# Kernel optimization log

Measured on AMD Instinct MI355X. Metric: run time of the kernel, lower is better.

The kernel has to match this reference:

```python
import jax, jax.numpy as jnp
import numpy as np

EPS = 1e-5

def _ln(x, g, b):
    mu = jnp.mean(x, axis=-1, keepdims=True)
    var = jnp.mean(jnp.square(x - mu), axis=-1, keepdims=True)
    return (x - mu) * jax.lax.rsqrt(var + EPS) * g + b

def setup_inputs() -> dict:
    B, T, D, E, H, M = 2, 2048, 1024, 8, 512, 2048
    key = jax.random.key(0)
    ks = jax.random.split(key, 24)
    s = 0.02
    inp = {}
    inp['x'] = jax.random.normal(ks[0], (B, T, D), jnp.float32)
    flat = jnp.arange(M, dtype=jnp.int32) * 2  # unique token ids over B*T
    inp['index_b'] = flat // T
    inp['index_t'] = flat % T
    # shared SwiGLU (hidden = H)
    inp['sw1'] = jax.random.normal(ks[1], (H, D), jnp.float32) * s
    inp['sb1'] = jnp.zeros((H,), jnp.float32)
    inp['sw2'] = jax.random.normal(ks[2], (H, D), jnp.float32) * s
    inp['sb2'] = jnp.zeros((H,), jnp.float32)
    inp['sw3'] = jax.random.normal(ks[3], (D, H), jnp.float32) * s
    inp['sb3'] = jnp.zeros((D,), jnp.float32)
    inp['s_ln_g'] = jnp.ones((H,), jnp.float32)
    inp['s_ln_b'] = jnp.zeros((H,), jnp.float32)
    # gates
    inp['sg_w'] = jax.random.normal(ks[4], (1, D), jnp.float32) * s
    inp['sg_b'] = jnp.zeros((1,), jnp.float32)
    inp['eg_w'] = jax.random.normal(ks[5], (E, D), jnp.float32) * s
    inp['eg_b'] = jnp.zeros((E,), jnp.float32)
    inp['exp_bias'] = jnp.zeros((E,), jnp.float32)
    # per-expert SwiGLU stacks
    inp['ew1'] = jax.random.normal(ks[6], (E, H, D), jnp.float32) * s
    inp['eb1'] = jnp.zeros((E, H), jnp.float32)
    inp['ew2'] = jax.random.normal(ks[7], (E, H, D), jnp.float32) * s
    inp['eb2'] = jnp.zeros((E, H), jnp.float32)
    inp['ew3'] = jax.random.normal(ks[8], (E, D, H), jnp.float32) * s
    inp['eb3'] = jnp.zeros((E, D), jnp.float32)
    inp['sel_ln_g'] = jnp.ones((H,), jnp.float32)
    inp['sel_ln_b'] = jnp.zeros((H,), jnp.float32)
    return inp

def _forward(x, index_b, index_t, sw1, sb1, sw2, sb2, sw3, sb3, s_ln_g, s_ln_b,
             sg_w, sg_b, eg_w, eg_b, exp_bias, ew1, eb1, ew2, eb2, ew3, eb3,
             sel_ln_g, sel_ln_b):
    # shared SwiGLU over all tokens: [B,T,D]
    x1 = jnp.einsum('btd,hd->bth', x, sw1) + sb1
    x2 = jnp.einsum('btd,hd->bth', x, sw2) + sb2
    sh = _ln(jax.nn.silu(x1) * x2, s_ln_g, s_ln_b)
    shared_out = jnp.einsum('bth,dh->btd', sh, sw3) + sb3
    # MoE tokens
    x_moe = x[index_b, index_t]  # [M,D]
    shared_scores = jax.nn.sigmoid(x_moe @ sg_w.T + sg_b)       # [M,1]
    expert_scores = jax.nn.sigmoid(x_moe @ eg_w.T + eg_b)       # [M,E]
    top1_idx = jnp.argmax(expert_scores + exp_bias, axis=-1)    # [M]
    top1_score = jnp.take_along_axis(expert_scores, top1_idx[:, None], axis=-1)  # [M,1]
    weights = jax.nn.softmax(jnp.concatenate([shared_scores, top1_score], axis=-1), axis=-1)
    shared_w, expert_w = weights[:, 0], weights[:, 1]
    shared_moe_out = shared_out[index_b, index_t] * shared_w[:, None]
    # per-expert SwiGLU computed densely for all E, then token selects its expert
    h1 = jnp.einsum('md,ehd->meh', x_moe, ew1) + eb1  # [M,E,H]
    h2 = jnp.einsum('md,ehd->meh', x_moe, ew2) + eb2
    z = _ln(jax.nn.silu(h1) * h2, sel_ln_g, sel_ln_b)
    out_all = jnp.einsum('meh,edh->med', z, ew3) + eb3  # [M,E,D]
    expert_out = jnp.take_along_axis(out_all, top1_idx[:, None, None], axis=1)[:, 0]  # [M,D]
    expert_moe_out = expert_out * expert_w[:, None]
    final_out = shared_out.at[index_b, index_t].set(shared_moe_out + expert_moe_out)
    return final_out

def reference(x, index_b, index_t, sw1, sb1, sw2, sb2, sw3, sb3, s_ln_g, s_ln_b,
              sg_w, sg_b, eg_w, eg_b, exp_bias, ew1, eb1, ew2, eb2, ew3, eb3,
              sel_ln_g, sel_ln_b):
    return _forward(x, index_b, index_t, sw1, sb1, sw2, sb2, sw3, sb3, s_ln_g, s_ln_b,
                    sg_w, sg_b, eg_w, eg_b, exp_bias, ew1, eb1, ew2, eb2, ew3, eb3,
                    sel_ln_g, sel_ln_b)
```

## Files before the change

kernel.cpp:

```cpp
#include <hip/hip_runtime.h>
#include <cstdint>

typedef unsigned short u16;
typedef __bf16 bf16x8 __attribute__((ext_vector_type(8)));
typedef float f32x4 __attribute__((ext_vector_type(4)));

#define T_SEQ  2048
#define D_DIM  1024
#define H_DIM  512
#define E_NUM  8
#define M_TOK  2048
#define BT_TOK 4096
#define MAXP   3072
#define NSPLIT_NONE (1 << 28)

static __device__ __forceinline__ u16 f2bf(float f) {
    union { float f; uint32_t u; } v; v.f = f;
    uint32_t u = v.u;
    return (u16)((u + 0x7FFFu + ((u >> 16) & 1u)) >> 16);
}
static __device__ __forceinline__ uint32_t pack2(float a, float b) {
    return (uint32_t)f2bf(a) | ((uint32_t)f2bf(b) << 16);
}

static __device__ __forceinline__ void gl_lds16(const u16* g, u16* l) {
    __builtin_amdgcn_global_load_lds(
        (const __attribute__((address_space(1))) uint32_t*)g,
        (__attribute__((address_space(3))) uint32_t*)l, 16, 0, 0);
}

__global__ __launch_bounds__(256)
void cvt_all_kernel(const float* __restrict__ x,
                    const float* __restrict__ sw1, const float* __restrict__ sw2,
                    const float* __restrict__ sw3,
                    const float* __restrict__ ew1, const float* __restrict__ ew2,
                    const float* __restrict__ ew3,
                    u16* __restrict__ xb,
                    u16* __restrict__ sw1b, u16* __restrict__ sw2b, u16* __restrict__ sw3b,
                    u16* __restrict__ ew1b, u16* __restrict__ ew2b, u16* __restrict__ ew3b)
{
    long i = (long)blockIdx.x * 256 + threadIdx.x;
    const float* s; u16* d; long off;
    if      (i < 1048576) { s = x;   d = xb;   off = i; }
    else if (i < 1179648) { s = sw1; d = sw1b; off = i - 1048576; }
    else if (i < 1310720) { s = sw2; d = sw2b; off = i - 1179648; }
    else if (i < 1441792) { s = sw3; d = sw3b; off = i - 1310720; }
    else if (i < 2490368) { s = ew1; d = ew1b; off = i - 1441792; }
    else if (i < 3538944) { s = ew2; d = ew2b; off = i - 2490368; }
    else                  { s = ew3; d = ew3b; off = i - 3538944; }
    float4 v = ((const float4*)s)[off];
    uint2 o;
    o.x = pack2(v.x, v.y);
    o.y = pack2(v.z, v.w);
    ((uint2*)d)[off] = o;
}


__device__ __forceinline__ void gating_body(
    int m,
    const float* __restrict__ x,
    const int* __restrict__ ib, const int* __restrict__ itx,
    const float* __restrict__ sgw, const float* __restrict__ sgb,
    const float* __restrict__ egw, const float* __restrict__ egb,
    const float* __restrict__ ebias,
    float* __restrict__ shw, float* __restrict__ expw,
    int* __restrict__ top1, int* __restrict__ rowidx,
    float* xs, float* sc)
{
    int tid = threadIdx.x;
    int row = ib[m] * T_SEQ + itx[m];
    if (tid == 0) rowidx[m] = row;
    const float* xr = x + (size_t)row * D_DIM;
    ((float4*)xs)[tid] = ((const float4*)xr)[tid];
    __syncthreads();
    int lane = tid & 63, w = tid >> 6;
    for (int sidx = w; sidx < 9; sidx += 4) {
        const float* wr = (sidx == 0) ? sgw : (egw + (size_t)(sidx - 1) * D_DIM);
        float acc = 0.f;
        for (int i = lane; i < D_DIM; i += 64) acc += xs[i] * wr[i];
        #pragma unroll
        for (int o = 32; o > 0; o >>= 1) acc += __shfl_xor(acc, o);
        if (lane == 0) sc[sidx] = acc;
    }
    __syncthreads();
    if (tid == 0) {
        float ss = 1.f / (1.f + expf(-(sc[0] + sgb[0])));
        float es[E_NUM];
        float best = -1e30f; int bi = 0;
        #pragma unroll
        for (int e = 0; e < E_NUM; ++e) {
            es[e] = 1.f / (1.f + expf(-(sc[1 + e] + egb[e])));
            float t = es[e] + ebias[e];
            if (t > best) { best = t; bi = e; }
        }
        float ts = es[bi];
        shw[m]  = 1.f / (1.f + expf(ts - ss));
        expw[m] = 1.f / (1.f + expf(ss - ts));
        top1[m] = bi;
    }
}

__device__ __forceinline__ void bucket_body(
    const int* __restrict__ top1,
    int* __restrict__ base, int* __restrict__ cnt, int* __restrict__ perm,
    int* sm)
{
    int* lc  = sm;
    int* lb  = sm + E_NUM;
    int* cur = sm + 2 * E_NUM + 1;
    int tid = threadIdx.x;
    if (tid < E_NUM) { lc[tid] = 0; cur[tid] = 0; }
    __syncthreads();
    for (int m = tid; m < M_TOK; m += 256) atomicAdd(&lc[top1[m]], 1);
    __syncthreads();
    if (tid == 0) {
        int bacc = 0;
        for (int e = 0; e < E_NUM; ++e) { lb[e] = bacc; bacc += (lc[e] + 63) & ~63; }
        lb[E_NUM] = bacc;
    }
    __syncthreads();
    for (int m = tid; m < M_TOK; m += 256) {
        int e = top1[m];
        int pos = lb[e] + atomicAdd(&cur[e], 1);
        perm[pos] = m;
    }
    if (tid <= E_NUM) base[tid] = lb[tid];
    if (tid < E_NUM)  cnt[tid]  = lc[tid];
}

template<bool SEL>
__device__ __forceinline__ void ln_body(
    int m,
    const float* __restrict__ X,
    const float* __restrict__ g, const float* __restrict__ b,
    u16* __restrict__ out,
    const int* __restrict__ base, const int* __restrict__ cnt,
    float* red)
{
    int tid = threadIdx.x;
    if (SEL) {
        bool valid = false;
        int tot = base[E_NUM];
        if (m < tot) {
            int e = 0;
            while (!(m >= base[e] && m < base[e + 1])) ++e;
            valid = (m - base[e]) < cnt[e];
        }
        if (!valid) {
            out[(size_t)m * H_DIM + tid] = 0;
            out[(size_t)m * H_DIM + tid + 256] = 0;
            return;
        }
    }
    const float* row = X + (size_t)m * D_DIM;
    float a0 = row[tid],       c0 = row[H_DIM + tid];
    float a1 = row[tid + 256], c1 = row[H_DIM + tid + 256];
    float v0 = (a0 / (1.f + expf(-a0))) * c0;
    float v1 = (a1 / (1.f + expf(-a1))) * c1;
    float s = v0 + v1, s2 = v0 * v0 + v1 * v1;
    #pragma unroll
    for (int o = 32; o > 0; o >>= 1) {
        s  += __shfl_xor(s, o);
        s2 += __shfl_xor(s2, o);
    }
    int w = tid >> 6;
    if ((tid & 63) == 0) { red[w] = s; red[4 + w] = s2; }
    __syncthreads();
    s  = red[0] + red[1] + red[2] + red[3];
    s2 = red[4] + red[5] + red[6] + red[7];
    float mu  = s * (1.f / H_DIM);
    float var = s2 * (1.f / H_DIM) - mu * mu;
    float inv = rsqrtf(var + 1e-5f);
    out[(size_t)m * H_DIM + tid]       = f2bf((v0 - mu) * inv * g[tid] + b[tid]);
    out[(size_t)m * H_DIM + tid + 256] = f2bf((v1 - mu) * inv * g[tid + 256] + b[tid + 256]);
}

template<int MODE, int KLEN>
__device__ __forceinline__ void gemm_body(
    int bn, int bm,
    const u16* __restrict__ A, int lda,
    const u16* __restrict__ W0, const u16* __restrict__ W1, int nsplit,
    const float* __restrict__ b0, const float* __restrict__ b1,
    float* __restrict__ C,
    const int* __restrict__ base, const int* __restrict__ cnt,
    const int* __restrict__ perm, const int* __restrict__ rowidx,
    const float* __restrict__ shw, const float* __restrict__ expw,
    u16* lds)
{
    constexpr int NITER = KLEN / 64;
    const int tid   = threadIdx.x;
    const int mbase = bm * 64;

    int pend = 0;
    if (MODE >= 2) {
        const int tot = base[E_NUM];
        if (mbase >= tot) return;
        int e = 0;
        while (!(mbase >= base[e] && mbase < base[e + 1])) ++e;
        pend = base[e] + cnt[e];
        if (mbase >= pend) return;
        const size_t wstride = (size_t)H_DIM * D_DIM;
        W0 += (size_t)e * wstride;
        if (MODE == 2) W1 += (size_t)e * wstride;
        b0 += e * ((MODE == 2) ? H_DIM : D_DIM);
        if (MODE == 2) b1 += e * H_DIM;
    }

    const int w  = tid >> 6;
    const int l  = tid & 63;
    const int sr = tid >> 3;
    const int sc = tid & 7;

    const u16* agp[2];
    #pragma unroll
    for (int t = 0; t < 2; ++t) {
        int r = t * 32 + sr;
        int grow;
        if (MODE == 2) {
            int p  = mbase + r;
            int pp = (p < pend) ? p : (pend - 1);
            grow = rowidx[perm[pp]];
        } else {
            grow = mbase + r;
        }
        agp[t] = A + (size_t)grow * lda + (sc ^ (r & 7)) * 8;
    }
    const u16* bgp[4];
    #pragma unroll
    for (int t = 0; t < 4; ++t) {
        int r = t * 32 + sr;
        int n = bn * 128 + r;
        bgp[t] = ((n < nsplit) ? (W0 + (size_t)n * KLEN)
                               : (W1 + (size_t)(n - nsplit) * KLEN)) + (sc ^ (r & 7)) * 8;
    }

    const int l16 = l & 15, quad = l >> 4;
    const int wm = w >> 1, wn = w & 1;

    int avo[2][2], bvo[4][2];
    #pragma unroll
    for (int i = 0; i < 2; ++i) {
        int R = wm * 32 + i * 16 + l16;
        #pragma unroll
        for (int kx = 0; kx < 2; ++kx)
            avo[i][kx] = R * 128 + (((kx * 4 + quad) ^ (R & 7)) * 16);
    }
    #pragma unroll
    for (int j = 0; j < 4; ++j) {
        int R = wn * 64 + j * 16 + l16;
        #pragma unroll
        for (int kx = 0; kx < 2; ++kx)
            bvo[j][kx] = 8192 + R * 128 + (((kx * 4 + quad) ^ (R & 7)) * 16);
    }

    f32x4 acc[2][4];
    #pragma unroll
    for (int i = 0; i < 2; ++i)
        #pragma unroll
        for (int j = 0; j < 4; ++j)
            acc[i][j] = (f32x4){0.f, 0.f, 0.f, 0.f};

    const int kstart = (bm + bn * 3) & (NITER - 1);
    const char* ldsc = (const char*)lds;

    for (int it = 0; it < NITER; ++it) {
        int k0 = ((it + kstart) & (NITER - 1)) * 64;
        #pragma unroll
        for (int t = 0; t < 2; ++t)
            gl_lds16(agp[t] + k0, lds + t * 2048 + w * 512);
        #pragma unroll
        for (int t = 0; t < 4; ++t)
            gl_lds16(bgp[t] + k0, lds + 4096 + t * 2048 + w * 512);
        __syncthreads();
        #pragma unroll
        for (int kx = 0; kx < 2; ++kx) {
            bf16x8 av[2], bv[4];
            #pragma unroll
            for (int i = 0; i < 2; ++i)
                av[i] = *(const bf16x8*)(ldsc + avo[i][kx]);
            #pragma unroll
            for (int j = 0; j < 4; ++j)
                bv[j] = *(const bf16x8*)(ldsc + bvo[j][kx]);
            #pragma unroll
            for (int i = 0; i < 2; ++i)
                #pragma unroll
                for (int j = 0; j < 4; ++j)
                    acc[i][j] = __builtin_amdgcn_mfma_f32_16x16x32_bf16(av[i], bv[j], acc[i][j], 0, 0, 0);
        }
        __syncthreads();
    }

    if (MODE == 3) {
        #pragma unroll
        for (int i = 0; i < 2; ++i) {
            #pragma unroll
            for (int rr = 0; rr < 4; ++rr) {
                int p = mbase + wm * 32 + i * 16 + quad * 4 + rr;
                if (p < pend) {
                    int tok = perm[p];
                    int row = rowidx[tok];
                    float sw = shw[tok], ew = expw[tok];
                    float* outr = C + (size_t)row * D_DIM;
                    #pragma unroll
                    for (int j = 0; j < 4; ++j) {
                        int gn = bn * 128 + wn * 64 + j * 16 + l16;
                        outr[gn] = outr[gn] * sw + (acc[i][j][rr] + b0[gn]) * ew;
                    }
                }
            }
        }
    } else {
        #pragma unroll
        for (int i = 0; i < 2; ++i) {
            #pragma unroll
            for (int rr = 0; rr < 4; ++rr) {
                int gm = mbase + wm * 32 + i * 16 + quad * 4 + rr;
                float* outr = C + (size_t)gm * D_DIM;
                #pragma unroll
                for (int j = 0; j < 4; ++j) {
                    int gn = bn * 128 + wn * 64 + j * 16 + l16;
                    float bias = (gn < nsplit) ? b0[gn] : b1[gn - nsplit];
                    outr[gn] = acc[i][j][rr] + bias;
                }
            }
        }
    }
}


__global__ __launch_bounds__(256, 4)
void k_g1_gating(const u16* __restrict__ xb,
                 const u16* __restrict__ sw1b, const u16* __restrict__ sw2b,
                 const float* __restrict__ sb1, const float* __restrict__ sb2,
                 float* __restrict__ x12,
                 const float* __restrict__ x,
                 const int* __restrict__ ib, const int* __restrict__ itx,
                 const float* __restrict__ sgw, const float* __restrict__ sgb,
                 const float* __restrict__ egw, const float* __restrict__ egb,
                 const float* __restrict__ ebias,
                 float* __restrict__ shw, float* __restrict__ expw,
                 int* __restrict__ top1, int* __restrict__ rowidx)
{
    __shared__ __align__(16) u16 lds[(64 + 128) * 64];
    int bx = blockIdx.x;
    if (bx < 512) {
        gemm_body<0, 1024>(bx & 7, bx >> 3, xb, D_DIM, sw1b, sw2b, H_DIM, sb1, sb2, x12,
                           nullptr, nullptr, nullptr, nullptr, nullptr, nullptr, lds);
    } else {
        float* xs = (float*)lds;
        float* sc = xs + D_DIM;
        gating_body(bx - 512, x, ib, itx, sgw, sgb, egw, egb, ebias,
                    shw, expw, top1, rowidx, xs, sc);
    }
}

__global__ __launch_bounds__(256)
void k_ln_bucket(const float* __restrict__ x12,
                 const float* __restrict__ g, const float* __restrict__ b,
                 u16* __restrict__ shn,
                 const int* __restrict__ top1,
                 int* __restrict__ basep, int* __restrict__ cntp, int* __restrict__ perm)
{
    __shared__ __align__(16) float smf[32];
    int bx = blockIdx.x;
    if (bx < BT_TOK) ln_body<false>(bx, x12, g, b, shn, nullptr, nullptr, smf);
    else             bucket_body(top1, basep, cntp, perm, (int*)smf);
}

__global__ __launch_bounds__(256, 4)
void k_g2_e1(const u16* __restrict__ shn, const u16* __restrict__ sw3b,
             const float* __restrict__ sb3, float* __restrict__ out,
             const u16* __restrict__ xb,
             const u16* __restrict__ ew1b, const u16* __restrict__ ew2b,
             const float* __restrict__ eb1, const float* __restrict__ eb2,
             float* __restrict__ h12,
             const int* __restrict__ basep, const int* __restrict__ cntp,
             const int* __restrict__ perm, const int* __restrict__ rowidx)
{
    __shared__ __align__(16) u16 lds[(64 + 128) * 64];
    int bx = blockIdx.x;
    if (bx < 512) {
        gemm_body<1, 512>(bx & 7, bx >> 3, shn, H_DIM, sw3b, sw3b, NSPLIT_NONE, sb3, sb3, out,
                          nullptr, nullptr, nullptr, nullptr, nullptr, nullptr, lds);
    } else {
        int b2 = bx - 512;
        gemm_body<2, 1024>(b2 & 7, b2 >> 3, xb, D_DIM, ew1b, ew2b, H_DIM, eb1, eb2, h12,
                           basep, cntp, perm, rowidx, nullptr, nullptr, lds);
    }
}

__global__ __launch_bounds__(256)
void k_ln_sel(const float* __restrict__ h12,
              const float* __restrict__ g, const float* __restrict__ b,
              u16* __restrict__ z,
              const int* __restrict__ basep, const int* __restrict__ cntp)
{
    __shared__ __align__(16) float smf[8];
    ln_body<true>(blockIdx.x, h12, g, b, z, basep, cntp, smf);
}

__global__ __launch_bounds__(256, 4)
void k_e2(const u16* __restrict__ z, const u16* __restrict__ ew3b,
          const float* __restrict__ eb3, float* __restrict__ out,
          const int* __restrict__ basep, const int* __restrict__ cntp,
          const int* __restrict__ perm, const int* __restrict__ rowidx,
          const float* __restrict__ shw, const float* __restrict__ expw)
{
    __shared__ __align__(16) u16 lds[(64 + 128) * 64];
    int bx = blockIdx.x;
    gemm_body<3, 512>(bx & 7, bx >> 3, z, H_DIM, ew3b, ew3b, NSPLIT_NONE, eb3, eb3, out,
                      basep, cntp, perm, rowidx, shw, expw, lds);
}

extern "C" void kernel_launch(void* const* d_in, const int* in_sizes, int n_in,
                              void* d_out, int out_size, void* d_ws, size_t ws_size,
                              hipStream_t stream) {
    const float* x        = (const float*)d_in[0];
    const int*   index_b  = (const int*)d_in[1];
    const int*   index_t  = (const int*)d_in[2];
    const float* sw1      = (const float*)d_in[3];
    const float* sb1      = (const float*)d_in[4];
    const float* sw2      = (const float*)d_in[5];
    const float* sb2      = (const float*)d_in[6];
    const float* sw3      = (const float*)d_in[7];
    const float* sb3      = (const float*)d_in[8];
    const float* s_ln_g   = (const float*)d_in[9];
    const float* s_ln_b   = (const float*)d_in[10];
    const float* sg_w     = (const float*)d_in[11];
    const float* sg_b     = (const float*)d_in[12];
    const float* eg_w     = (const float*)d_in[13];
    const float* eg_b     = (const float*)d_in[14];
    const float* exp_bias = (const float*)d_in[15];
    const float* ew1      = (const float*)d_in[16];
    const float* eb1      = (const float*)d_in[17];
    const float* ew2      = (const float*)d_in[18];
    const float* eb2      = (const float*)d_in[19];
    const float* ew3      = (const float*)d_in[20];
    const float* eb3      = (const float*)d_in[21];
    const float* sel_ln_g = (const float*)d_in[22];
    const float* sel_ln_b = (const float*)d_in[23];
    float* out = (float*)d_out;
    char*  ws  = (char*)d_ws;

    u16*   xb   = (u16*)(ws + 0);
    u16*   sw1b = (u16*)(ws + 8388608);
    u16*   sw2b = (u16*)(ws + 9437184);
    u16*   sw3b = (u16*)(ws + 10485760);
    u16*   ew1b = (u16*)(ws + 11534336);
    u16*   ew2b = (u16*)(ws + 19922944);
    u16*   ew3b = (u16*)(ws + 28311552);
    float* x12  = (float*)(ws + 36700160);
    float* h12  = x12;
    u16*   sh   = (u16*)(ws + 53477376);
    u16*   z    = sh;
    float* shw    = (float*)(ws + 57671680);
    float* expw   = shw + M_TOK;
    int*   top1   = (int*)(expw + M_TOK);
    int*   rowidx = top1 + M_TOK;
    int*   perm   = rowidx + M_TOK;
    int*   basep  = perm + MAXP;
    int*   cntp   = basep + 16;

    cvt_all_kernel<<<dim3(17920), dim3(256), 0, stream>>>(
        x, sw1, sw2, sw3, ew1, ew2, ew3,
        xb, sw1b, sw2b, sw3b, ew1b, ew2b, ew3b);

    k_g1_gating<<<dim3(512 + M_TOK), dim3(256), 0, stream>>>(
        xb, sw1b, sw2b, sb1, sb2, x12,
        x, index_b, index_t, sg_w, sg_b, eg_w, eg_b, exp_bias,
        shw, expw, top1, rowidx);

    k_ln_bucket<<<dim3(BT_TOK + 1), dim3(256), 0, stream>>>(
        x12, s_ln_g, s_ln_b, sh, top1, basep, cntp, perm);

    k_g2_e1<<<dim3(512 + 8 * (MAXP / 64)), dim3(256), 0, stream>>>(
        sh, sw3b, sb3, out,
        xb, ew1b, ew2b, eb1, eb2, h12,
        basep, cntp, perm, rowidx);

    k_ln_sel<<<dim3(MAXP), dim3(256), 0, stream>>>(
        h12, sel_ln_g, sel_ln_b, z, basep, cntp);

    k_e2<<<dim3(8 * (MAXP / 64)), dim3(256), 0, stream>>>(
        z, ew3b, eb3, out, basep, cntp, perm, rowidx, shw, expw);
}
```

Before: 236.8 us.

## Double-buffer GEMM LDS tiles and regroup gating, conversion and bucketing launches

```diff
diff --git a/kernel.cpp b/kernel.cpp
--- a/kernel.cpp
+++ b/kernel.cpp
@@ -27,32 +27,6 @@
     __builtin_amdgcn_global_load_lds(
         (const __attribute__((address_space(1))) uint32_t*)g,
         (__attribute__((address_space(3))) uint32_t*)l, 16, 0, 0);
-}
-
-__global__ __launch_bounds__(256)
-void cvt_all_kernel(const float* __restrict__ x,
-                    const float* __restrict__ sw1, const float* __restrict__ sw2,
-                    const float* __restrict__ sw3,
-                    const float* __restrict__ ew1, const float* __restrict__ ew2,
-                    const float* __restrict__ ew3,
-                    u16* __restrict__ xb,
-                    u16* __restrict__ sw1b, u16* __restrict__ sw2b, u16* __restrict__ sw3b,
-                    u16* __restrict__ ew1b, u16* __restrict__ ew2b, u16* __restrict__ ew3b)
-{
-    long i = (long)blockIdx.x * 256 + threadIdx.x;
-    const float* s; u16* d; long off;
-    if      (i < 1048576) { s = x;   d = xb;   off = i; }
-    else if (i < 1179648) { s = sw1; d = sw1b; off = i - 1048576; }
-    else if (i < 1310720) { s = sw2; d = sw2b; off = i - 1179648; }
-    else if (i < 1441792) { s = sw3; d = sw3b; off = i - 1310720; }
-    else if (i < 2490368) { s = ew1; d = ew1b; off = i - 1441792; }
-    else if (i < 3538944) { s = ew2; d = ew2b; off = i - 2490368; }
-    else                  { s = ew3; d = ew3b; off = i - 3538944; }
-    float4 v = ((const float4*)s)[off];
-    uint2 o;
-    o.x = pack2(v.x, v.y);
-    o.y = pack2(v.z, v.w);
-    ((uint2*)d)[off] = o;
 }
 
 
@@ -263,31 +237,46 @@
     const int kstart = (bm + bn * 3) & (NITER - 1);
     const char* ldsc = (const char*)lds;
 
-    for (int it = 0; it < NITER; ++it) {
-        int k0 = ((it + kstart) & (NITER - 1)) * 64;
+    {
+        int k0 = (kstart & (NITER - 1)) * 64;
         #pragma unroll
         for (int t = 0; t < 2; ++t)
             gl_lds16(agp[t] + k0, lds + t * 2048 + w * 512);
         #pragma unroll
         for (int t = 0; t < 4; ++t)
             gl_lds16(bgp[t] + k0, lds + 4096 + t * 2048 + w * 512);
-        __syncthreads();
+    }
+    __syncthreads();
+
+    for (int it = 0; it < NITER; ++it) {
+        const int cur = it & 1;
+        if (it + 1 < NITER) {
+            int k0 = ((it + 1 + kstart) & (NITER - 1)) * 64;
+            u16* lb = lds + (cur ^ 1) * 12288;
+            #pragma unroll
+            for (int t = 0; t < 2; ++t)
+                gl_lds16(agp[t] + k0, lb + t * 2048 + w * 512);
+            #pragma unroll
+            for (int t = 0; t < 4; ++t)
+                gl_lds16(bgp[t] + k0, lb + 4096 + t * 2048 + w * 512);
+        }
+        const char* lb = ldsc + cur * 24576;
         #pragma unroll
         for (int kx = 0; kx < 2; ++kx) {
             bf16x8 av[2], bv[4];
             #pragma unroll
             for (int i = 0; i < 2; ++i)
-                av[i] = *(const bf16x8*)(ldsc + avo[i][kx]);
+                av[i] = *(const bf16x8*)(lb + avo[i][kx]);
             #pragma unroll
             for (int j = 0; j < 4; ++j)
-                bv[j] = *(const bf16x8*)(ldsc + bvo[j][kx]);
+                bv[j] = *(const bf16x8*)(lb + bvo[j][kx]);
             #pragma unroll
             for (int i = 0; i < 2; ++i)
                 #pragma unroll
                 for (int j = 0; j < 4; ++j)
                     acc[i][j] = __builtin_amdgcn_mfma_f32_16x16x32_bf16(av[i], bv[j], acc[i][j], 0, 0, 0);
         }
-        __syncthreads();
+        if (it + 1 < NITER) __syncthreads();
     }
 
     if (MODE == 3) {
@@ -328,43 +317,70 @@
 }
 
 
+__global__ __launch_bounds__(256)
+void k_cvt_gating(const float* __restrict__ x,
+                  const float* __restrict__ sw1, const float* __restrict__ sw2,
+                  const float* __restrict__ sw3,
+                  const float* __restrict__ ew1, const float* __restrict__ ew2,
+                  const float* __restrict__ ew3,
+                  u16* __restrict__ xb,
+                  u16* __restrict__ sw1b, u16* __restrict__ sw2b, u16* __restrict__ sw3b,
+                  u16* __restrict__ ew1b, u16* __restrict__ ew2b, u16* __restrict__ ew3b,
+                  const int* __restrict__ ib, const int* __restrict__ itx,
+                  const float* __restrict__ sgw, const float* __restrict__ sgb,
+                  const float* __restrict__ egw, const float* __restrict__ egb,
+                  const float* __restrict__ ebias,
+                  float* __restrict__ shw, float* __restrict__ expw,
+                  int* __restrict__ top1, int* __restrict__ rowidx)
+{
+    __shared__ __align__(16) float smem[D_DIM + 16];
+    int bx = blockIdx.x;
+    if (bx < M_TOK) {
+        gating_body(bx, x, ib, itx, sgw, sgb, egw, egb, ebias,
+                    shw, expw, top1, rowidx, smem, smem + D_DIM);
+        return;
+    }
+    long i = (long)(bx - M_TOK) * 256 + threadIdx.x;
+    const float* s; u16* d; long off;
+    if      (i < 1048576) { s = x;   d = xb;   off = i; }
+    else if (i < 1179648) { s = sw1; d = sw1b; off = i - 1048576; }
+    else if (i < 1310720) { s = sw2; d = sw2b; off = i - 1179648; }
+    else if (i < 1441792) { s = sw3; d = sw3b; off = i - 1310720; }
+    else if (i < 2490368) { s = ew1; d = ew1b; off = i - 1441792; }
+    else if (i < 3538944) { s = ew2; d = ew2b; off = i - 2490368; }
+    else                  { s = ew3; d = ew3b; off = i - 3538944; }
+    float4 v = ((const float4*)s)[off];
+    uint2 o;
+    o.x = pack2(v.x, v.y);
+    o.y = pack2(v.z, v.w);
+    ((uint2*)d)[off] = o;
+}
+
 __global__ __launch_bounds__(256, 4)
-void k_g1_gating(const u16* __restrict__ xb,
+void k_g1_bucket(const u16* __restrict__ xb,
                  const u16* __restrict__ sw1b, const u16* __restrict__ sw2b,
                  const float* __restrict__ sb1, const float* __restrict__ sb2,
                  float* __restrict__ x12,
-                 const float* __restrict__ x,
-                 const int* __restrict__ ib, const int* __restrict__ itx,
-                 const float* __restrict__ sgw, const float* __restrict__ sgb,
-                 const float* __restrict__ egw, const float* __restrict__ egb,
-                 const float* __restrict__ ebias,
-                 float* __restrict__ shw, float* __restrict__ expw,
-                 int* __restrict__ top1, int* __restrict__ rowidx)
-{
-    __shared__ __align__(16) u16 lds[(64 + 128) * 64];
+                 const int* __restrict__ top1,
+                 int* __restrict__ basep, int* __restrict__ cntp, int* __restrict__ perm)
+{
+    __shared__ __align__(16) u16 lds[2 * (64 + 128) * 64];
     int bx = blockIdx.x;
     if (bx < 512) {
         gemm_body<0, 1024>(bx & 7, bx >> 3, xb, D_DIM, sw1b, sw2b, H_DIM, sb1, sb2, x12,
                            nullptr, nullptr, nullptr, nullptr, nullptr, nullptr, lds);
     } else {
-        float* xs = (float*)lds;
-        float* sc = xs + D_DIM;
-        gating_body(bx - 512, x, ib, itx, sgw, sgb, egw, egb, ebias,
-                    shw, expw, top1, rowidx, xs, sc);
+        bucket_body(top1, basep, cntp, perm, (int*)lds);
     }
 }
 
 __global__ __launch_bounds__(256)
-void k_ln_bucket(const float* __restrict__ x12,
-                 const float* __restrict__ g, const float* __restrict__ b,
-                 u16* __restrict__ shn,
-                 const int* __restrict__ top1,
-                 int* __restrict__ basep, int* __restrict__ cntp, int* __restrict__ perm)
-{
-    __shared__ __align__(16) float smf[32];
-    int bx = blockIdx.x;
-    if (bx < BT_TOK) ln_body<false>(bx, x12, g, b, shn, nullptr, nullptr, smf);
-    else             bucket_body(top1, basep, cntp, perm, (int*)smf);
+void k_ln(const float* __restrict__ x12,
+          const float* __restrict__ g, const float* __restrict__ b,
+          u16* __restrict__ shn)
+{
+    __shared__ __align__(16) float smf[8];
+    ln_body<false>(blockIdx.x, x12, g, b, shn, nullptr, nullptr, smf);
 }
 
 __global__ __launch_bounds__(256, 4)
@@ -377,7 +393,7 @@
              const int* __restrict__ basep, const int* __restrict__ cntp,
              const int* __restrict__ perm, const int* __restrict__ rowidx)
 {
-    __shared__ __align__(16) u16 lds[(64 + 128) * 64];
+    __shared__ __align__(16) u16 lds[2 * (64 + 128) * 64];
     int bx = blockIdx.x;
     if (bx < 512) {
         gemm_body<1, 512>(bx & 7, bx >> 3, shn, H_DIM, sw3b, sw3b, NSPLIT_NONE, sb3, sb3, out,
@@ -406,7 +422,7 @@
           const int* __restrict__ perm, const int* __restrict__ rowidx,
           const float* __restrict__ shw, const float* __restrict__ expw)
 {
-    __shared__ __align__(16) u16 lds[(64 + 128) * 64];
+    __shared__ __align__(16) u16 lds[2 * (64 + 128) * 64];
     int bx = blockIdx.x;
     gemm_body<3, 512>(bx & 7, bx >> 3, z, H_DIM, ew3b, ew3b, NSPLIT_NONE, eb3, eb3, out,
                       basep, cntp, perm, rowidx, shw, expw, lds);
@@ -461,17 +477,16 @@
     int*   basep  = perm + MAXP;
     int*   cntp   = basep + 16;
 
-    cvt_all_kernel<<<dim3(17920), dim3(256), 0, stream>>>(
+    k_cvt_gating<<<dim3(M_TOK + 17920), dim3(256), 0, stream>>>(
         x, sw1, sw2, sw3, ew1, ew2, ew3,
-        xb, sw1b, sw2b, sw3b, ew1b, ew2b, ew3b);
-
-    k_g1_gating<<<dim3(512 + M_TOK), dim3(256), 0, stream>>>(
-        xb, sw1b, sw2b, sb1, sb2, x12,
-        x, index_b, index_t, sg_w, sg_b, eg_w, eg_b, exp_bias,
+        xb, sw1b, sw2b, sw3b, ew1b, ew2b, ew3b,
+        index_b, index_t, sg_w, sg_b, eg_w, eg_b, exp_bias,
         shw, expw, top1, rowidx);
 
-    k_ln_bucket<<<dim3(BT_TOK + 1), dim3(256), 0, stream>>>(
-        x12, s_ln_g, s_ln_b, sh, top1, basep, cntp, perm);
+    k_g1_bucket<<<dim3(512 + 1), dim3(256), 0, stream>>>(
+        xb, sw1b, sw2b, sb1, sb2, x12, top1, basep, cntp, perm);
+
+    k_ln<<<dim3(BT_TOK), dim3(256), 0, stream>>>(x12, s_ln_g, s_ln_b, sh);
 
     k_g2_e1<<<dim3(512 + 8 * (MAXP / 64)), dim3(256), 0, stream>>>(
         sh, sw3b, sb3, out,
```

After: 231.9 us. 1.02x faster.
